# Kernel optimization log

Hardware: AMD Instinct MI355X
Metric: run time of the kernel (lower is better)

The kernel has to match this reference:

```python
import jax, jax.numpy as jnp
import numpy as np

D_MODEL = 256
NHEAD = 8
NUM_EXPERTS = 5
LQ, LK, BATCH = 100, 1024, 16
LN_EPS = 1e-5


def setup_inputs() -> dict:
    key = jax.random.key(0)
    ks = jax.random.split(key, 12)
    d, E = D_MODEL, NUM_EXPERTS
    s = 1.0 / np.sqrt(d)
    return {
        "tgt": jax.random.normal(ks[0], (LQ, BATCH, d), jnp.float32),
        "memory": jax.random.normal(ks[1], (LK, BATCH, d), jnp.float32),
        "query_pos": jax.random.normal(ks[2], (LQ, BATCH, d), jnp.float32),
        "pos": jax.random.normal(ks[3], (LK, BATCH, d), jnp.float32),
        # per-expert MultiheadAttention params (packed q,k,v in_proj like torch)
        "w_in": jax.random.normal(ks[4], (E, 3 * d, d), jnp.float32) * s,
        "b_in": jnp.zeros((E, 3 * d), jnp.float32),
        "w_out": jax.random.normal(ks[5], (E, d, d), jnp.float32) * s,
        "b_out": jnp.zeros((E, d), jnp.float32),
        # gating network
        "w_gate": jax.random.normal(ks[6], (E, d), jnp.float32) * s,
        "b_gate": jnp.zeros((E,), jnp.float32),
        # LayerNorm
        "ln_gamma": jnp.ones((d,), jnp.float32),
        "ln_beta": jnp.zeros((d,), jnp.float32),
    }


def _moe_cross_attn(tgt, memory, query_pos, pos, w_in, b_in, w_out, b_out,
                    w_gate, b_gate, ln_gamma, ln_beta):
    Lq, B, d = tgt.shape
    H = NHEAD
    hd = d // H
    E = w_in.shape[0]
    Lk = memory.shape[0]

    # gating over (seq*batch, d) -> softmax over experts
    gate = jax.nn.softmax(tgt @ w_gate.T + b_gate, axis=-1)  # (Lq, B, E)

    q_emb = tgt + query_pos      # (Lq, B, d)
    k_emb = memory + pos         # (Lk, B, d)

    wq, wk, wv = w_in[:, :d], w_in[:, d:2 * d], w_in[:, 2 * d:]
    bq, bk, bv = b_in[:, :d], b_in[:, d:2 * d], b_in[:, 2 * d:]

    # batched projections across all experts (replaces python loop of MHA calls)
    q = jnp.einsum('lbd,eod->elbo', q_emb, wq) + bq[:, None, None, :]
    k = jnp.einsum('sbd,eod->esbo', k_emb, wk) + bk[:, None, None, :]
    v = jnp.einsum('sbd,eod->esbo', memory, wv) + bv[:, None, None, :]

    q = q.reshape(E, Lq, B, H, hd) * (1.0 / np.sqrt(hd))
    k = k.reshape(E, Lk, B, H, hd)
    v = v.reshape(E, Lk, B, H, hd)

    scores = jnp.einsum('elbhk,esbhk->ebhls', q, k)      # (E, B, H, Lq, Lk)
    attn = jax.nn.softmax(scores, axis=-1)
    ctx = jnp.einsum('ebhls,esbhk->elbhk', attn, v).reshape(E, Lq, B, d)

    out = jnp.einsum('elbd,eod->elbo', ctx, w_out) + b_out[:, None, None, :]

    # softmax-gated weighted combine of expert outputs
    mo = jnp.einsum('lbe,elbd->lbd', gate, out)

    x = tgt + mo  # dropout is identity (p=0.0)
    mu = jnp.mean(x, axis=-1, keepdims=True)
    var = jnp.var(x, axis=-1, keepdims=True)
    return (x - mu) * jax.lax.rsqrt(var + LN_EPS) * ln_gamma + ln_beta


def reference(tgt, memory, query_pos, pos, w_in, b_in, w_out, b_out,
              w_gate, b_gate, ln_gamma, ln_beta):
    return _moe_cross_attn(tgt, memory, query_pos, pos, w_in, b_in, w_out,
                           b_out, w_gate, b_gate, ln_gamma, ln_beta)
```

## Files before the change

### kernel.cpp

```cpp
#include <hip/hip_runtime.h>


typedef __bf16 bf16x8 __attribute__((ext_vector_type(8)));
typedef float f32x4 __attribute__((ext_vector_type(4)));
typedef unsigned int u32x4 __attribute__((ext_vector_type(4)));
typedef unsigned int u32x2 __attribute__((ext_vector_type(2)));
typedef unsigned short u16x4 __attribute__((ext_vector_type(4)));
typedef unsigned short us;

__device__ __forceinline__ us f2bf(float f) {
    unsigned u = __builtin_bit_cast(unsigned, f);
    u += 0x7FFFu + ((u >> 16) & 1u);
    return (us)(u >> 16);
}

__device__ __forceinline__ unsigned pack2(float lo, float hi) {
    return (unsigned)f2bf(lo) | ((unsigned)f2bf(hi) << 16);
}

__device__ __forceinline__ float bf2f(us v) {
    unsigned u = ((unsigned)v) << 16;
    return __builtin_bit_cast(float, u);
}

__device__ __forceinline__ bf16x8 ld_bf8(const us* p) {
    return __builtin_bit_cast(bf16x8, *reinterpret_cast<const u32x4*>(p));
}

__device__ __forceinline__ void gld_lds16(const us* g, us* l) {
    __builtin_amdgcn_global_load_lds(
        (const __attribute__((address_space(1))) unsigned int*)g,
        (__attribute__((address_space(3))) unsigned int*)l, 16, 0, 0);
}

__launch_bounds__(256)
__global__ void cvt_all(const float* __restrict__ tgt, const float* __restrict__ qpos,
                        const float* __restrict__ mem, const float* __restrict__ pos,
                        const float* __restrict__ w_in, const float* __restrict__ w_out,
                        us* __restrict__ Aq, us* __restrict__ Ak, us* __restrict__ Av,
                        us* __restrict__ Wb, us* __restrict__ WOb)
{
    const int bid = blockIdx.x;
    const int tid = threadIdx.x;
    if (bid < 400) {
        int i = bid * 256 + tid;
        f32x4 a = reinterpret_cast<const f32x4*>(tgt)[i];
        f32x4 b = reinterpret_cast<const f32x4*>(qpos)[i];
        u16x4 r;
#pragma unroll
        for (int j = 0; j < 4; ++j) r[j] = f2bf(a[j] + b[j]);
        reinterpret_cast<u16x4*>(Aq)[i] = r;
    } else if (bid < 4496) {
        int i = (bid - 400) * 256 + tid;
        f32x4 m = reinterpret_cast<const f32x4*>(mem)[i];
        f32x4 p = reinterpret_cast<const f32x4*>(pos)[i];
        u16x4 rk, rv;
#pragma unroll
        for (int j = 0; j < 4; ++j) { rk[j] = f2bf(m[j] + p[j]); rv[j] = f2bf(m[j]); }
        reinterpret_cast<u16x4*>(Ak)[i] = rk;
        reinterpret_cast<u16x4*>(Av)[i] = rv;
    } else if (bid < 5456) {
        int i = (bid - 4496) * 256 + tid;
        f32x4 a = reinterpret_cast<const f32x4*>(w_in)[i];
        u16x4 r;
#pragma unroll
        for (int j = 0; j < 4; ++j) r[j] = f2bf(a[j]);
        reinterpret_cast<u16x4*>(Wb)[i] = r;
    } else {
        int i = (bid - 5456) * 256 + tid;
        f32x4 a = reinterpret_cast<const f32x4*>(w_out)[i];
        u16x4 r;
#pragma unroll
        for (int j = 0; j < 4; ++j) r[j] = f2bf(a[j]);
        reinterpret_cast<u16x4*>(WOb)[i] = r;
    }
}

template <bool BF16OUT>
__device__ __forceinline__ void gemm_body(const us* __restrict__ A,
                                          const us* __restrict__ W,
                                          const float* __restrict__ bias,
                                          void* __restrict__ Cout,
                                          float scale, int M)
{
    const int row0 = blockIdx.x * 128;
    const int col0 = blockIdx.y * 128;
    __shared__ us As[2 * 8192];
    __shared__ us Bs[2 * 8192];
    const int tid  = threadIdx.x;
    const int lane = tid & 63;
    const int w    = tid >> 6;
    const int l15  = lane & 15;
    const int quad = lane >> 4;
    const int wm   = (w >> 1) * 64;
    const int wn   = (w & 1) * 64;
    const int srow = lane >> 3;
    const int gofs = ((lane & 7) ^ srow) * 8;

#pragma unroll
    for (int cc = 0; cc < 4; ++cc) {
        const int c = w * 4 + cc;
        const int row = c * 8 + srow;
        gld_lds16(A + (size_t)(row0 + row) * 256 + gofs, &As[c * 512]);
        gld_lds16(W + (size_t)(col0 + row) * 256 + gofs, &Bs[c * 512]);
    }
    __syncthreads();

    f32x4 acc[4][4] = {};

#pragma unroll
    for (int kt = 0; kt < 4; ++kt) {
        const int cur = (kt & 1) * 8192;
        if (kt < 3) {
            const int nxt = ((kt + 1) & 1) * 8192;
            const int k0 = (kt + 1) * 64;
#pragma unroll
            for (int cc = 0; cc < 4; ++cc) {
                const int c = w * 4 + cc;
                const int row = c * 8 + srow;
                gld_lds16(A + (size_t)(row0 + row) * 256 + k0 + gofs, &As[nxt + c * 512]);
                gld_lds16(W + (size_t)(col0 + row) * 256 + k0 + gofs, &Bs[nxt + c * 512]);
            }
        }
#pragma unroll
        for (int kh = 0; kh < 2; ++kh) {
            bf16x8 af[4], bf[4];
#pragma unroll
            for (int mi = 0; mi < 4; ++mi) {
                const int row = wm + mi * 16 + l15;
                const int seg = (kh * 4 + quad) ^ (row & 7);
                af[mi] = ld_bf8(&As[cur + row * 64 + seg * 8]);
            }
#pragma unroll
            for (int ni = 0; ni < 4; ++ni) {
                const int col = wn + ni * 16 + l15;
                const int seg = (kh * 4 + quad) ^ (col & 7);
                bf[ni] = ld_bf8(&Bs[cur + col * 64 + seg * 8]);
            }
#pragma unroll
            for (int mi = 0; mi < 4; ++mi)
#pragma unroll
                for (int ni = 0; ni < 4; ++ni)
                    acc[mi][ni] = __builtin_amdgcn_mfma_f32_16x16x32_bf16(bf[ni], af[mi], acc[mi][ni], 0, 0, 0);
        }
        if (kt < 3) __syncthreads();
    }

#pragma unroll
    for (int mi = 0; mi < 4; ++mi) {
        const int row = row0 + wm + mi * 16 + l15;
        if (row < M) {
#pragma unroll
            for (int ni = 0; ni < 4; ++ni) {
                const int colb = col0 + wn + ni * 16 + quad * 4;
                const f32x4 b4 = *reinterpret_cast<const f32x4*>(bias + colb);
                if constexpr (BF16OUT) {
                    u32x2 pk;
                    pk[0] = pack2((acc[mi][ni][0] + b4[0]) * scale,
                                  (acc[mi][ni][1] + b4[1]) * scale);
                    pk[1] = pack2((acc[mi][ni][2] + b4[2]) * scale,
                                  (acc[mi][ni][3] + b4[3]) * scale);
                    *reinterpret_cast<u32x2*>(reinterpret_cast<us*>(Cout) + (size_t)row * 256 + colb) = pk;
                } else {
                    f32x4 v;
#pragma unroll
                    for (int r = 0; r < 4; ++r) v[r] = (acc[mi][ni][r] + b4[r]) * scale;
                    *reinterpret_cast<f32x4*>(reinterpret_cast<float*>(Cout) + (size_t)row * 256 + colb) = v;
                }
            }
        }
    }
}

__launch_bounds__(256)
__global__ void gemm_qkv(const us* __restrict__ Aq, const us* __restrict__ Ak,
                         const us* __restrict__ Av, const us* __restrict__ Wb,
                         const float* __restrict__ b_in,
                         us* __restrict__ Qb, us* __restrict__ Kb, us* __restrict__ Vb)
{
    const int z = blockIdx.z;
    if (z < 5) {
        if (blockIdx.x >= 13) return;
        gemm_body<true>(Aq, Wb + (size_t)z * 196608, b_in + (size_t)z * 768,
                        Qb + (size_t)z * 409600, 0.17677669529663687f, 1600);
    } else if (z < 10) {
        const int e = z - 5;
        gemm_body<true>(Ak, Wb + 65536 + (size_t)e * 196608, b_in + (size_t)e * 768 + 256,
                        Kb + (size_t)e * 4194304, 1.0f, 16384);
    } else {
        const int e = z - 10;
        gemm_body<true>(Av, Wb + 131072 + (size_t)e * 196608, b_in + (size_t)e * 768 + 512,
                        Vb + (size_t)e * 4194304, 1.0f, 16384);
    }
}

__launch_bounds__(256)
__global__ void gemm_o(const us* __restrict__ CTXb, const us* __restrict__ WOb,
                       const float* __restrict__ b_out, float* __restrict__ OUTf)
{
    const int e = blockIdx.z;
    gemm_body<false>(CTXb + (size_t)e * 409600, WOb + (size_t)e * 65536,
                     b_out + (size_t)e * 256, OUTf + (size_t)e * 409600, 1.0f, 1600);
}

__device__ __forceinline__ int vrow(int d) { return d * 264 + 8 * (d >> 3); }

__launch_bounds__(512)
__global__ void attn(const us* __restrict__ Qb, const us* __restrict__ Kb,
                     const us* __restrict__ Vb, us* __restrict__ PO,
                     float* __restrict__ PL)
{
    const int h = blockIdx.x;
    const int z = blockIdx.y;
    const int s = blockIdx.z;
    const int e = z >> 4, b = z & 15;
    const int tid  = threadIdx.x;
    const int w    = tid >> 6;
    const int lane = tid & 63;
    const int l15  = lane & 15, quad = lane >> 4;
    __shared__ us Ks[256 * 32];
    __shared__ us Vs[8464];
    __shared__ us Ps[7][16 * 40];

    const int key0 = s * 256;
    {
        const int kl  = lane >> 2;
        const int seg = lane & 3;
        const us* kg = Kb + ((size_t)((e * 1024 + key0 + w * 16 + kl) * 16 + b)) * 256
                          + h * 32 + seg * 8;
        gld_lds16(kg, &Ks[w * 512]);
        gld_lds16(kg + (size_t)128 * 16 * 256, &Ks[4096 + w * 512]);

        const int kv = tid >> 2;
        const int sg = tid & 3;
        const us* vg = Vb + ((size_t)((e * 1024 + key0 + kv) * 16 + b)) * 256
                          + h * 32 + sg * 8;
        u32x4 v0 = *reinterpret_cast<const u32x4*>(vg);
        u32x4 v1 = *reinterpret_cast<const u32x4*>(vg + (size_t)128 * 16 * 256);
#pragma unroll
        for (int j = 0; j < 4; ++j) {
            const int d0 = sg * 8 + 2 * j;
            const int e0 = vrow(d0);
            const int e1 = e0 + 264;
            Vs[e0 + kv]       = (us)(v0[j] & 0xffff);
            Vs[e1 + kv]       = (us)(v0[j] >> 16);
            Vs[e0 + 128 + kv] = (us)(v1[j] & 0xffff);
            Vs[e1 + 128 + kv] = (us)(v1[j] >> 16);
        }
    }
    u32x4 qraw = {0u, 0u, 0u, 0u};
    if (w < 7) {
        const int l = w * 16 + l15;
        if (l < 100)
            qraw = *reinterpret_cast<const u32x4*>(
                Qb + ((size_t)((e * 100 + l) * 16 + b)) * 256 + h * 32 + quad * 8);
    }
    const bf16x8 qf = __builtin_bit_cast(bf16x8, qraw);

    __syncthreads();

    if (w >= 7) return;

    const f32x4 zacc = {};
    f32x4 o0 = {}, o1 = {};
    float lsum = 0.0f;

    for (int c = 0; c < 8; ++c) {
        bf16x8 kf0 = ld_bf8(&Ks[(c * 32 + l15) * 32 + quad * 8]);
        bf16x8 kf1 = ld_bf8(&Ks[(c * 32 + 16 + l15) * 32 + quad * 8]);
        f32x4 s0 = __builtin_amdgcn_mfma_f32_16x16x32_bf16(kf0, qf, zacc, 0, 0, 0);
        f32x4 s1 = __builtin_amdgcn_mfma_f32_16x16x32_bf16(kf1, qf, zacc, 0, 0, 0);
        float p0[4], p1[4];
#pragma unroll
        for (int r = 0; r < 4; ++r) {
            p0[r] = __expf(s0[r]);
            p1[r] = __expf(s1[r]);
            lsum += p0[r] + p1[r];
        }
        u32x2 w0, w1;
        w0[0] = pack2(p0[0], p0[1]);
        w0[1] = pack2(p0[2], p0[3]);
        w1[0] = pack2(p1[0], p1[1]);
        w1[1] = pack2(p1[2], p1[3]);
        *reinterpret_cast<u32x2*>(&Ps[w][l15 * 40 + quad * 4])      = w0;
        *reinterpret_cast<u32x2*>(&Ps[w][l15 * 40 + 16 + quad * 4]) = w1;
        bf16x8 pf  = ld_bf8(&Ps[w][l15 * 40 + quad * 8]);
        bf16x8 vf0 = ld_bf8(&Vs[vrow(l15) + c * 32 + quad * 8]);
        bf16x8 vf1 = ld_bf8(&Vs[vrow(16 + l15) + c * 32 + quad * 8]);
        o0 = __builtin_amdgcn_mfma_f32_16x16x32_bf16(pf, vf0, o0, 0, 0, 0);
        o1 = __builtin_amdgcn_mfma_f32_16x16x32_bf16(pf, vf1, o1, 0, 0, 0);
    }

    lsum += __shfl_xor(lsum, 16, 64);
    lsum += __shfl_xor(lsum, 32, 64);

#pragma unroll
    for (int r = 0; r < 4; ++r) {
        const int row = w * 16 + quad * 4 + r;
        if (row < 100) {
            const size_t o = (((size_t)((s * 5 + e) * 100 + row)) * 16 + b) * 256 + h * 32;
            PO[o + l15]      = f2bf(o0[r]);
            PO[o + 16 + l15] = f2bf(o1[r]);
        }
    }
    const int q = w * 16 + l15;
    if (quad == 0 && q < 100)
        PL[((((size_t)s * 5 + e) * 16 + b) * 8 + h) * 128 + q] = lsum;
}

__launch_bounds__(256)
__global__ void combine(const us* __restrict__ PO, const float* __restrict__ PL,
                        us* __restrict__ CTX)
{
    const int blk = blockIdx.x;
    const int e   = blk / 1600;
    const int rem = blk - e * 1600;
    const int row = rem >> 4;
    const int b   = rem & 15;
    const int d   = threadIdx.x;
    const int h   = d >> 5;
    float O = 0.0f, L = 0.0f;
#pragma unroll
    for (int s = 0; s < 4; ++s) {
        O += bf2f(PO[(((size_t)((s * 5 + e) * 100 + row)) * 16 + b) * 256 + d]);
        L += PL[((((size_t)s * 5 + e) * 16 + b) * 8 + h) * 128 + row];
    }
    CTX[(((size_t)(e * 100 + row)) * 16 + b) * 256 + d] = f2bf(O / L);
}

__launch_bounds__(256)
__global__ void finalize(const float* __restrict__ tgt, const float* __restrict__ w_gate,
                         const float* __restrict__ b_gate, const float* __restrict__ OUTf,
                         const float* __restrict__ gamma, const float* __restrict__ beta,
                         float* __restrict__ out)
{
    const int row = blockIdx.x;
    const int d = threadIdx.x;
    __shared__ float red[4];
    const float t = tgt[(size_t)row * 256 + d];

    float g[5];
#pragma unroll
    for (int e = 0; e < 5; ++e) {
        float part = t * w_gate[e * 256 + d];
#pragma unroll
        for (int off = 32; off >= 1; off >>= 1) part += __shfl_xor(part, off, 64);
        if ((d & 63) == 0) red[d >> 6] = part;
        __syncthreads();
        g[e] = red[0] + red[1] + red[2] + red[3] + b_gate[e];
        __syncthreads();
    }
    float mx = g[0];
#pragma unroll
    for (int e = 1; e < 5; ++e) mx = fmaxf(mx, g[e]);
    float sm = 0.0f;
#pragma unroll
    for (int e = 0; e < 5; ++e) { g[e] = __expf(g[e] - mx); sm += g[e]; }
    const float invs = 1.0f / sm;

    float mo = 0.0f;
#pragma unroll
    for (int e = 0; e < 5; ++e)
        mo += g[e] * invs * OUTf[((size_t)e * 1600 + row) * 256 + d];
    const float x = t + mo;

    float part = x;
#pragma unroll
    for (int off = 32; off >= 1; off >>= 1) part += __shfl_xor(part, off, 64);
    if ((d & 63) == 0) red[d >> 6] = part;
    __syncthreads();
    const float mean = (red[0] + red[1] + red[2] + red[3]) * (1.0f / 256.0f);
    __syncthreads();

    const float diff = x - mean;
    part = diff * diff;
#pragma unroll
    for (int off = 32; off >= 1; off >>= 1) part += __shfl_xor(part, off, 64);
    if ((d & 63) == 0) red[d >> 6] = part;
    __syncthreads();
    const float var = (red[0] + red[1] + red[2] + red[3]) * (1.0f / 256.0f);

    out[(size_t)row * 256 + d] = diff * rsqrtf(var + 1e-5f) * gamma[d] + beta[d];
}

extern "C" void kernel_launch(void* const* d_in, const int* in_sizes, int n_in,
                              void* d_out, int out_size, void* d_ws, size_t ws_size,
                              hipStream_t stream)
{
    const float* tgt    = (const float*)d_in[0];
    const float* mem    = (const float*)d_in[1];
    const float* qpos   = (const float*)d_in[2];
    const float* pos    = (const float*)d_in[3];
    const float* w_in   = (const float*)d_in[4];
    const float* b_in   = (const float*)d_in[5];
    const float* w_out  = (const float*)d_in[6];
    const float* b_out  = (const float*)d_in[7];
    const float* w_gate = (const float*)d_in[8];
    const float* b_gate = (const float*)d_in[9];
    const float* ln_g   = (const float*)d_in[10];
    const float* ln_b   = (const float*)d_in[11];
    float* out = (float*)d_out;

    char* p = (char*)d_ws;
    auto alloc = [&](size_t n) { char* r = p; p += (n + 255) & ~(size_t)255; return r; };

    us* Aq   = (us*)alloc(409600ull * 2);
    us* Ak   = (us*)alloc(4194304ull * 2);
    us* Av   = (us*)alloc(4194304ull * 2);
    us* Wb   = (us*)alloc(983040ull * 2);
    us* WOb  = (us*)alloc(327680ull * 2);
    us* Qb   = (us*)alloc(5ull * 409600 * 2);
    us* Kb   = (us*)alloc(5ull * 4194304 * 2);
    us* Vb   = (us*)alloc(5ull * 4194304 * 2);
    us* CTXb = (us*)alloc(5ull * 409600 * 2);
    float* OUTf = (float*)alloc(5ull * 409600 * 4);
    us*    PO = (us*)d_ws;
    float* PL = (float*)((char*)d_ws + 16384000);

    cvt_all<<<5776, 256, 0, stream>>>(tgt, qpos, mem, pos, w_in, w_out,
                                      Aq, Ak, Av, Wb, WOb);

    gemm_qkv<<<dim3(128, 2, 15), 256, 0, stream>>>(Aq, Ak, Av, Wb, b_in, Qb, Kb, Vb);

    attn<<<dim3(8, 80, 4), 512, 0, stream>>>(Qb, Kb, Vb, PO, PL);

    combine<<<8000, 256, 0, stream>>>(PO, PL, CTXb);

    gemm_o<<<dim3(13, 2, 5), 256, 0, stream>>>(CTXb, WOb, b_out, OUTf);

    finalize<<<1600, 256, 0, stream>>>(tgt, w_gate, b_gate, OUTf, ln_g, ln_b, out);
}
```

Baseline: 213.1 us.

## Fuse split-K combine into output GEMM and move gating into convert kernel

Removes the separate combine kernel. The output-projection GEMM now reads the four split partial outputs and their softmax denominators directly, normalizes them, and writes the result into shared memory as its A operand. Gate softmax is computed once per row inside the convert kernel and stored. Finalize then uses a single-pass mean/variance reduction with fewer barriers. This saves one launch and the CTX round trip through memory, at the cost of a heavier A-load path in the GEMM and a slightly less stable variance formula.

```diff
diff --git a/kernel.cpp b/kernel.cpp
--- a/kernel.cpp
+++ b/kernel.cpp
@@ -37,19 +37,43 @@
 __global__ void cvt_all(const float* __restrict__ tgt, const float* __restrict__ qpos,
                         const float* __restrict__ mem, const float* __restrict__ pos,
                         const float* __restrict__ w_in, const float* __restrict__ w_out,
+                        const float* __restrict__ w_gate, const float* __restrict__ b_gate,
                         us* __restrict__ Aq, us* __restrict__ Ak, us* __restrict__ Av,
-                        us* __restrict__ Wb, us* __restrict__ WOb)
+                        us* __restrict__ Wb, us* __restrict__ WOb,
+                        float* __restrict__ Gate)
 {
     const int bid = blockIdx.x;
     const int tid = threadIdx.x;
     if (bid < 400) {
-        int i = bid * 256 + tid;
+        const int i = bid * 256 + tid;
+        const int lane = tid & 63;
+        const int row = i >> 6;
         f32x4 a = reinterpret_cast<const f32x4*>(tgt)[i];
         f32x4 b = reinterpret_cast<const f32x4*>(qpos)[i];
         u16x4 r;
 #pragma unroll
         for (int j = 0; j < 4; ++j) r[j] = f2bf(a[j] + b[j]);
         reinterpret_cast<u16x4*>(Aq)[i] = r;
+        float g[5];
+#pragma unroll
+        for (int e = 0; e < 5; ++e) {
+            f32x4 wg = *reinterpret_cast<const f32x4*>(w_gate + e * 256 + 4 * lane);
+            float p = a[0] * wg[0] + a[1] * wg[1] + a[2] * wg[2] + a[3] * wg[3];
+#pragma unroll
+            for (int off = 32; off >= 1; off >>= 1) p += __shfl_xor(p, off, 64);
+            g[e] = p + b_gate[e];
+        }
+        float mx = g[0];
+#pragma unroll
+        for (int e = 1; e < 5; ++e) mx = fmaxf(mx, g[e]);
+        float sm = 0.0f;
+#pragma unroll
+        for (int e = 0; e < 5; ++e) { g[e] = __expf(g[e] - mx); sm += g[e]; }
+        const float invs = 1.0f / sm;
+        if (lane == 0) {
+#pragma unroll
+            for (int e = 0; e < 5; ++e) Gate[row * 5 + e] = g[e] * invs;
+        }
     } else if (bid < 4496) {
         int i = (bid - 400) * 256 + tid;
         f32x4 m = reinterpret_cast<const f32x4*>(mem)[i];
@@ -195,12 +219,136 @@
 }
 
 __launch_bounds__(256)
-__global__ void gemm_o(const us* __restrict__ CTXb, const us* __restrict__ WOb,
-                       const float* __restrict__ b_out, float* __restrict__ OUTf)
+__global__ void gemm_og(const us* __restrict__ PO, const float* __restrict__ PL,
+                        const us* __restrict__ WOb, const float* __restrict__ b_out,
+                        float* __restrict__ OUTf)
 {
     const int e = blockIdx.z;
-    gemm_body<false>(CTXb + (size_t)e * 409600, WOb + (size_t)e * 65536,
-                     b_out + (size_t)e * 256, OUTf + (size_t)e * 409600, 1.0f, 1600);
+    const us* W = WOb + (size_t)e * 65536;
+    const float* bias = b_out + (size_t)e * 256;
+    float* Cout = OUTf + (size_t)e * 409600;
+
+    const int row0 = blockIdx.x * 128;
+    const int col0 = blockIdx.y * 128;
+    __shared__ us As[2 * 8192];
+    __shared__ us Bs[2 * 8192];
+    const int tid  = threadIdx.x;
+    const int lane = tid & 63;
+    const int w    = tid >> 6;
+    const int l15  = lane & 15;
+    const int quad = lane >> 4;
+    const int wm   = (w >> 1) * 64;
+    const int wn   = (w & 1) * 64;
+    const int srow = lane >> 3;
+    const int gofs = ((lane & 7) ^ srow) * 8;
+
+    u32x4 POr[4][4];
+    float Lr[4];
+
+    auto loadA = [&](int kt) {
+#pragma unroll
+        for (int cc = 0; cc < 4; ++cc) {
+            const int c = w * 4 + cc;
+            int grow = row0 + c * 8 + srow;
+            if (grow > 1599) grow = 1599;
+            const int d0 = kt * 64 + gofs;
+            const size_t base = (size_t)e * 409600 + (size_t)grow * 256 + d0;
+#pragma unroll
+            for (int s = 0; s < 4; ++s)
+                POr[cc][s] = *reinterpret_cast<const u32x4*>(PO + base + (size_t)s * 2048000);
+            const int l = grow >> 4, bb = grow & 15, h = d0 >> 5;
+            float L = 0.0f;
+#pragma unroll
+            for (int s = 0; s < 4; ++s)
+                L += PL[((((size_t)s * 5 + e) * 16 + bb) * 8 + h) * 128 + l];
+            Lr[cc] = L;
+        }
+    };
+    auto writeA = [&](int buf) {
+#pragma unroll
+        for (int cc = 0; cc < 4; ++cc) {
+            const float inv = 1.0f / Lr[cc];
+            u32x4 pk;
+#pragma unroll
+            for (int j = 0; j < 4; ++j) {
+                float v0 = 0.0f, v1 = 0.0f;
+#pragma unroll
+                for (int s = 0; s < 4; ++s) {
+                    const unsigned u = POr[cc][s][j];
+                    v0 += __builtin_bit_cast(float, u << 16);
+                    v1 += __builtin_bit_cast(float, u & 0xffff0000u);
+                }
+                pk[j] = pack2(v0 * inv, v1 * inv);
+            }
+            *reinterpret_cast<u32x4*>(&As[buf * 8192 + (w * 4 + cc) * 512 + lane * 8]) = pk;
+        }
+    };
+    auto loadW = [&](int buf, int kt) {
+#pragma unroll
+        for (int cc = 0; cc < 4; ++cc) {
+            const int c = w * 4 + cc;
+            const int row = c * 8 + srow;
+            gld_lds16(W + (size_t)(col0 + row) * 256 + kt * 64 + gofs,
+                      &Bs[buf * 8192 + c * 512]);
+        }
+    };
+
+    loadA(0);
+    loadW(0, 0);
+    writeA(0);
+    __syncthreads();
+
+    f32x4 acc[4][4] = {};
+
+#pragma unroll
+    for (int kt = 0; kt < 4; ++kt) {
+        const int cur = kt & 1;
+        if (kt < 3) {
+            loadA(kt + 1);
+            loadW(cur ^ 1, kt + 1);
+        }
+#pragma unroll
+        for (int kh = 0; kh < 2; ++kh) {
+            bf16x8 af[4], bf[4];
+#pragma unroll
+            for (int mi = 0; mi < 4; ++mi) {
+                const int row = wm + mi * 16 + l15;
+                const int seg = (kh * 4 + quad) ^ (row & 7);
+                af[mi] = ld_bf8(&As[cur * 8192 + row * 64 + seg * 8]);
+            }
+#pragma unroll
+            for (int ni = 0; ni < 4; ++ni) {
+                const int col = wn + ni * 16 + l15;
+                const int seg = (kh * 4 + quad) ^ (col & 7);
+                bf[ni] = ld_bf8(&Bs[cur * 8192 + col * 64 + seg * 8]);
+            }
+#pragma unroll
+            for (int mi = 0; mi < 4; ++mi)
+#pragma unroll
+                for (int ni = 0; ni < 4; ++ni)
+                    acc[mi][ni] = __builtin_amdgcn_mfma_f32_16x16x32_bf16(bf[ni], af[mi], acc[mi][ni], 0, 0, 0);
+        }
+        if (kt < 3) {
+            writeA(cur ^ 1);
+            __syncthreads();
+        }
+    }
+
+#pragma unroll
+    for (int mi = 0; mi < 4; ++mi) {
+        const int row = row0 + wm + mi * 16 + l15;
+        if (row < 1600) {
+#pragma unroll
+            for (int ni = 0; ni < 4; ++ni) {
+                const int colb = col0 + wn + ni * 16 + quad * 4;
+                const f32x4 b4 = *reinterpret_cast<const f32x4*>(bias + colb);
+                f32x4 v;
+#pragma unroll
+                for (int r = 0; r < 4; ++r) v[r] = acc[mi][ni][r] + b4[r];
+                *reinterpret_cast<f32x4*>(Cout + (size_t)row * 256 + colb) = v;
+            }
+        }
+    }
 }
 
 __device__ __forceinline__ int vrow(int d) { return d * 264 + 8 * (d >> 3); }
@@ -309,78 +457,35 @@
 }
 
 __launch_bounds__(256)
-__global__ void combine(const us* __restrict__ PO, const float* __restrict__ PL,
-                        us* __restrict__ CTX)
-{
-    const int blk = blockIdx.x;
-    const int e   = blk / 1600;
-    const int rem = blk - e * 1600;
-    const int row = rem >> 4;
-    const int b   = rem & 15;
-    const int d   = threadIdx.x;
-    const int h   = d >> 5;
-    float O = 0.0f, L = 0.0f;
-#pragma unroll
-    for (int s = 0; s < 4; ++s) {
-        O += bf2f(PO[(((size_t)((s * 5 + e) * 100 + row)) * 16 + b) * 256 + d]);
-        L += PL[((((size_t)s * 5 + e) * 16 + b) * 8 + h) * 128 + row];
-    }
-    CTX[(((size_t)(e * 100 + row)) * 16 + b) * 256 + d] = f2bf(O / L);
-}
-
-__launch_bounds__(256)
-__global__ void finalize(const float* __restrict__ tgt, const float* __restrict__ w_gate,
-                         const float* __restrict__ b_gate, const float* __restrict__ OUTf,
+__global__ void finalize(const float* __restrict__ tgt, const float* __restrict__ Gate,
+                         const float* __restrict__ OUTf,
                          const float* __restrict__ gamma, const float* __restrict__ beta,
                          float* __restrict__ out)
 {
     const int row = blockIdx.x;
     const int d = threadIdx.x;
-    __shared__ float red[4];
+    __shared__ float red[8];
     const float t = tgt[(size_t)row * 256 + d];
 
-    float g[5];
-#pragma unroll
-    for (int e = 0; e < 5; ++e) {
-        float part = t * w_gate[e * 256 + d];
-#pragma unroll
-        for (int off = 32; off >= 1; off >>= 1) part += __shfl_xor(part, off, 64);
-        if ((d & 63) == 0) red[d >> 6] = part;
-        __syncthreads();
-        g[e] = red[0] + red[1] + red[2] + red[3] + b_gate[e];
-        __syncthreads();
-    }
-    float mx = g[0];
-#pragma unroll
-    for (int e = 1; e < 5; ++e) mx = fmaxf(mx, g[e]);
-    float sm = 0.0f;
-#pragma unroll
-    for (int e = 0; e < 5; ++e) { g[e] = __expf(g[e] - mx); sm += g[e]; }
-    const float invs = 1.0f / sm;
-
     float mo = 0.0f;
 #pragma unroll
     for (int e = 0; e < 5; ++e)
-        mo += g[e] * invs * OUTf[((size_t)e * 1600 + row) * 256 + d];
+        mo += Gate[row * 5 + e] * OUTf[((size_t)e * 1600 + row) * 256 + d];
     const float x = t + mo;
 
-    float part = x;
-#pragma unroll
-    for (int off = 32; off >= 1; off >>= 1) part += __shfl_xor(part, off, 64);
-    if ((d & 63) == 0) red[d >> 6] = part;
+    float p1 = x, p2 = x * x;
+#pragma unroll
+    for (int off = 32; off >= 1; off >>= 1) {
+        p1 += __shfl_xor(p1, off, 64);
+        p2 += __shfl_xor(p2, off, 64);
+    }
+    if ((d & 63) == 0) { red[d >> 6] = p1; red[4 + (d >> 6)] = p2; }
     __syncthreads();
     const float mean = (red[0] + red[1] + red[2] + red[3]) * (1.0f / 256.0f);
-    __syncthreads();
-
-    const float diff = x - mean;
-    part = diff * diff;
-#pragma unroll
-    for (int off = 32; off >= 1; off >>= 1) part += __shfl_xor(part, off, 64);
-    if ((d & 63) == 0) red[d >> 6] = part;
-    __syncthreads();
-    const float var = (red[0] + red[1] + red[2] + red[3]) * (1.0f / 256.0f);
-
-    out[(size_t)row * 256 + d] = diff * rsqrtf(var + 1e-5f) * gamma[d] + beta[d];
+    const float msq  = (red[4] + red[5] + red[6] + red[7]) * (1.0f / 256.0f);
+    const float var  = msq - mean * mean;
+
+    out[(size_t)row * 256 + d] = (x - mean) * rsqrtf(var + 1e-5f) * gamma[d] + beta[d];
 }
 
 extern "C" void kernel_launch(void* const* d_in, const int* in_sizes, int n_in,
@@ -412,21 +517,19 @@
     us* Qb   = (us*)alloc(5ull * 409600 * 2);
     us* Kb   = (us*)alloc(5ull * 4194304 * 2);
     us* Vb   = (us*)alloc(5ull * 4194304 * 2);
-    us* CTXb = (us*)alloc(5ull * 409600 * 2);
-    float* OUTf = (float*)alloc(5ull * 409600 * 4);
+    float* OUTf  = (float*)alloc(5ull * 409600 * 4);
+    float* Gate  = (float*)alloc(1600ull * 5 * 4);
     us*    PO = (us*)d_ws;
     float* PL = (float*)((char*)d_ws + 16384000);
 
     cvt_all<<<5776, 256, 0, stream>>>(tgt, qpos, mem, pos, w_in, w_out,
-                                      Aq, Ak, Av, Wb, WOb);
+                                      w_gate, b_gate, Aq, Ak, Av, Wb, WOb, Gate);
 
     gemm_qkv<<<dim3(128, 2, 15), 256, 0, stream>>>(Aq, Ak, Av, Wb, b_in, Qb, Kb, Vb);
 
     attn<<<dim3(8, 80, 4), 512, 0, stream>>>(Qb, Kb, Vb, PO, PL);
 
-    combine<<<8000, 256, 0, stream>>>(PO, PL, CTXb);
-
-    gemm_o<<<dim3(13, 2, 5), 256, 0, stream>>>(CTXb, WOb, b_out, OUTf);
-
-    finalize<<<1600, 256, 0, stream>>>(tgt, w_gate, b_gate, OUTf, ln_g, ln_b, out);
-}
+    gemm_og<<<dim3(13, 2, 5), 256, 0, stream>>>(PO, PL, WOb, b_out, OUTf);
+
+    finalize<<<1600, 256, 0, stream>>>(tgt, Gate, OUTf, ln_g, ln_b, out);
+}
```

New measurement: 210.1 us. About the same (-1.4%).
